# Performance work log

Measured on AMD Instinct MI355X. Metric: run time of the kernel, lower is better.

## Reference

```python
import jax, jax.numpy as jnp
import numpy as np

EMBEDDING_DIM = 256
NUM_EMBEDDINGS = 2048
COMMITMENT_COST = 0.25


def setup_inputs() -> dict:
    key = jax.random.key(0)
    k1, k2 = jax.random.split(key)
    inputs = jax.random.normal(k1, (32, EMBEDDING_DIM, 32, 32), dtype=jnp.float32)
    # learned codebook buffer, shape (D, K) as in the torch module
    embedding = jax.random.normal(k2, (EMBEDDING_DIM, NUM_EMBEDDINGS), dtype=jnp.float32)
    return {"inputs": inputs, "embedding": embedding}


def reference(inputs, embedding):
    # Eval-mode forward of VectorQuantizerEMA (EMA buffer updates are
    # training-only side effects and do not affect the returned values).
    B, D, H, W = inputs.shape
    K = embedding.shape[1]
    x = inputs.astype(jnp.float32)
    # (B, D, H, W) -> (N, D), N = B*H*W, clamped as in the source
    flat = jnp.clip(jnp.transpose(x, (0, 2, 3, 1)).reshape(-1, D), -10.0, 10.0)
    # squared L2 distances to every codeword: (N, K)
    distances = (
        jnp.sum(flat * flat, axis=1, keepdims=True)
        + jnp.sum(embedding * embedding, axis=0, keepdims=True)
        - 2.0 * (flat @ embedding)
    )
    encoding_indices = jnp.argmin(distances, axis=1)  # (N,)
    # one-hot @ emb.T is just a gather of codebook columns
    q_flat = jnp.take(embedding.T, encoding_indices, axis=0)  # (N, D)
    quantized = jnp.transpose(q_flat.reshape(B, H, W, D), (0, 3, 1, 2))
    # VQ losses (computed against the un-clamped float inputs, as in torch)
    e_latent_loss = jnp.mean((jax.lax.stop_gradient(quantized) - x) ** 2)
    q_latent_loss = jnp.mean((quantized - jax.lax.stop_gradient(x)) ** 2)
    loss = q_latent_loss + COMMITMENT_COST * e_latent_loss
    # straight-through estimator
    quantized_st = inputs + jax.lax.stop_gradient(quantized - inputs)
    # perplexity from codeword usage (mean one-hot == normalized counts)
    n = encoding_indices.shape[0]
    avg_probs = jnp.zeros((K,), dtype=jnp.float32).at[encoding_indices].add(1.0) / n
    perplexity = jnp.exp(-jnp.sum(avg_probs * jnp.log(avg_probs + 1e-10)))
    return quantized_st, loss, perplexity, encoding_indices
```

## Files before the change

kernel.cpp:

```cpp
#include <hip/hip_runtime.h>
#include <hip/hip_bf16.h>
#include <math.h>

typedef unsigned int  uint;
typedef unsigned short ushort;

#define DD    256
#define KK    2048
#define HW    1024
#define NN    32768
#define NUMEL 8388608
#define STRIDEB (DD*HW)
#define NBLK_QL (NUMEL/1024)

#define WS_H2     0
#define WS_COUNTS 8192
#define WS_LOSS   16384
#define WS_EBF    16512
#define WS_PV     2113664
#define WS_PI     2375808
#define WS_BPART  WS_PV

#define OUT_LOSS  8388608
#define OUT_PPL   8388609
#define OUT_IDX   8388610

typedef __attribute__((ext_vector_type(8))) short  short8;
typedef __attribute__((ext_vector_type(4))) float  float4v;

typedef __attribute__((address_space(1))) uint guint;
typedef __attribute__((address_space(3))) uint luint;

__device__ __forceinline__ ushort f2bf(float f) {
    uint u = __float_as_uint(f);
    return (ushort)((u + 0x7FFFu + ((u >> 16) & 1u)) >> 16);
}

__global__ __launch_bounds__(256) void e2h_kernel(const float* __restrict__ emb,
                                                  float* __restrict__ h2,
                                                  int*   __restrict__ counts) {
    int k = blockIdx.x * 256 + threadIdx.x;
    float s = 0.f;
    for (int d = 0; d < DD; ++d) {
        float v = emb[(size_t)d * KK + k];
        s += v * v;
    }
    h2[k] = 0.5f * s;
    counts[k] = 0;
}

__global__ __launch_bounds__(256) void prep_emb(const float* __restrict__ emb,
                                                ushort* __restrict__ ebf) {
    int g  = blockIdx.x * 256 + threadIdx.x;
    int k  = g & (KK - 1);
    int dg = g >> 11;
    int d0 = dg * 8;
    int s    = dg >> 2;
    int quad = dg & 3;
    int ct   = k >> 4;
    int l    = quad * 16 + (k & 15);

    union { ushort us[8]; uint4 v; } hu, lu;
#pragma unroll
    for (int j = 0; j < 8; ++j) {
        float v = emb[(size_t)(d0 + j) * KK + k];
        ushort hb = f2bf(v);
        float  hf = __uint_as_float(((uint)hb) << 16);
        hu.us[j] = hb;
        lu.us[j] = f2bf(v - hf);
    }
    size_t hi_off = (size_t)(((ct * 8 + s) * 2 + 0) * 64 + l) * 8;
    size_t lo_off = (size_t)(((ct * 8 + s) * 2 + 1) * 64 + l) * 8;
    *(uint4*)(ebf + hi_off) = hu.v;
    *(uint4*)(ebf + lo_off) = lu.v;
}

__global__ __launch_bounds__(256, 4) void argmin_mfma(
    const float*  __restrict__ x,
    const ushort* __restrict__ ebf,
    const float*  __restrict__ h2,
    float* __restrict__ pv,
    int*   __restrict__ pi)
{
    __shared__ ushort sB[2][8192];
    __shared__ float  sH2[1024];

    const int tid  = threadIdx.x;
    const int w    = tid >> 6;
    const int lane = tid & 63;
    const int m    = lane & 15;
    const int quad = lane >> 4;

    const int rb = blockIdx.x >> 1;
    const int ch = blockIdx.x & 1;
    const int n0 = rb * 64 + w * 16;
    const int b  = n0 >> 10;
    const int hwb = n0 & 1023;
    const float* xb = x + (size_t)b * STRIDEB;
    const int cbase = ch * 1024;
    const int ctg0  = cbase >> 4;

    auto stage = [&](ushort* dst, int ctg) {
        const char* gs = (const char*)(ebf + (size_t)ctg * 8192) + tid * 16;
        char*       ls = (char*)dst + tid * 16;
#pragma unroll
        for (int i = 0; i < 4; ++i)
            __builtin_amdgcn_global_load_lds((guint*)(gs + i * 4096),
                                             (luint*)(ls + i * 4096),
                                             16, 0, 0);
    };

    stage(sB[0], ctg0);
    ((float4*)sH2)[tid] = ((const float4*)(h2 + cbase))[tid];

    short8 xh[8], xl[8];
    {
        const int hw = hwb + m;
#pragma unroll
        for (int s = 0; s < 8; ++s) {
            const float* p = xb + (size_t)(s * 32 + quad * 8) * HW + hw;
            short8 hh, ll;
#pragma unroll
            for (int j = 0; j < 8; ++j) {
                float v = p[(size_t)j * HW];
                v = fminf(fmaxf(v, -10.f), 10.f);
                ushort hb = f2bf(v);
                float  hf = __uint_as_float(((uint)hb) << 16);
                hh[j] = (short)hb;
                ll[j] = (short)f2bf(v - hf);
            }
            xh[s] = hh;
            xl[s] = ll;
        }
    }

    float bv[4] = {1e30f, 1e30f, 1e30f, 1e30f};
    int   bi[4] = {0, 0, 0, 0};

    auto compute_tile = [&](const ushort* sbc, int ct) {
        float4v accA = {0,0,0,0}, accB = {0,0,0,0};
#pragma unroll
        for (int s = 0; s < 8; ++s) {
            short8 eh = *(const short8*)&sbc[(s * 2 + 0) * 512 + lane * 8];
            short8 el = *(const short8*)&sbc[(s * 2 + 1) * 512 + lane * 8];
            accB = __builtin_amdgcn_mfma_f32_16x16x32_bf16(xl[s], eh, accB, 0, 0, 0);
            accB = __builtin_amdgcn_mfma_f32_16x16x32_bf16(xh[s], el, accB, 0, 0, 0);
            accA = __builtin_amdgcn_mfma_f32_16x16x32_bf16(xh[s], eh, accA, 0, 0, 0);
        }
        const int c  = cbase + ct * 16 + m;
        const float hv = sH2[ct * 16 + m];
#pragma unroll
        for (int i = 0; i < 4; ++i) {
            float s0 = hv - (accA[i] + accB[i]);
            if (s0 < bv[i]) { bv[i] = s0; bi[i] = c; }
        }
    };

    __syncthreads();

    for (int ct = 0; ct < 64; ct += 2) {
        stage(sB[1], ctg0 + ct + 1);
        compute_tile(sB[0], ct);
        __syncthreads();
        stage(sB[0], (ct + 2 < 64) ? (ctg0 + ct + 2) : ctg0);
        compute_tile(sB[1], ct + 1);
        __syncthreads();
    }

#pragma unroll
    for (int i = 0; i < 4; ++i) {
        float v  = bv[i];
        int   ix = bi[i];
#pragma unroll
        for (int msk = 8; msk >= 1; msk >>= 1) {
            float ov = __shfl_xor(v, msk, 64);
            int   oi = __shfl_xor(ix, msk, 64);
            if (ov < v || (ov == v && oi < ix)) { v = ov; ix = oi; }
        }
        if (m == 0) {
            int n = n0 + quad * 4 + i;
            pv[n * 2 + ch] = v;
            pi[n * 2 + ch] = ix;
        }
    }
}

__global__ __launch_bounds__(256) void merge_kernel(
    const float* __restrict__ pv, const int* __restrict__ pi,
    float* __restrict__ out_idx_f, int* __restrict__ counts)
{
    int n = blockIdx.x * 256 + threadIdx.x;
    float v0 = pv[n * 2 + 0], v1 = pv[n * 2 + 1];
    int   i0 = pi[n * 2 + 0], i1 = pi[n * 2 + 1];
    int ix = (v1 < v0) ? i1 : i0;
    ix = min(max(ix, 0), KK - 1);
    out_idx_f[n] = (float)ix;
    atomicAdd(&counts[ix], 1);
}

__global__ __launch_bounds__(256) void quant_loss_kernel(
    const float* __restrict__ x,
    const float* __restrict__ emb,
    const float* __restrict__ idxf,
    float* __restrict__ outq,
    float* __restrict__ bpart)
{
    __shared__ float red[4];
    size_t o4 = ((size_t)blockIdx.x * 256 + threadIdx.x) * 4;
    int b  = (int)(o4 >> 18);
    int d  = (int)((o4 >> 10) & 255);
    int n  = b * HW + (int)(o4 & 1023);
    int i0 = (int)idxf[n + 0];
    int i1 = (int)idxf[n + 1];
    int i2 = (int)idxf[n + 2];
    int i3 = (int)idxf[n + 3];
    i0 = min(max(i0, 0), KK - 1); i1 = min(max(i1, 0), KK - 1);
    i2 = min(max(i2, 0), KK - 1); i3 = min(max(i3, 0), KK - 1);
    const float* er = emb + (size_t)d * KK;
    float4 q;
    q.x = er[i0]; q.y = er[i1]; q.z = er[i2]; q.w = er[i3];
    const float4 xv = *(const float4*)(x + o4);
    *(float4*)(outq + o4) = q;
    float ax = q.x - xv.x, ay = q.y - xv.y, az = q.z - xv.z, aw = q.w - xv.w;
    float s = ax * ax + ay * ay + az * az + aw * aw;
#pragma unroll
    for (int off = 32; off > 0; off >>= 1) s += __shfl_down(s, off, 64);
    if ((threadIdx.x & 63) == 0) red[threadIdx.x >> 6] = s;
    __syncthreads();
    if (threadIdx.x == 0)
        bpart[blockIdx.x] = red[0] + red[1] + red[2] + red[3];
}

__global__ __launch_bounds__(256) void finalize_kernel(
    const int* __restrict__ counts,
    const float* __restrict__ bpart,
    float* __restrict__ out)
{
    __shared__ float redp[4], redl[4];
    int tid = threadIdx.x;
    float s = 0.f;
    for (int k = tid; k < KK; k += 256) {
        float p = (float)counts[k] * (1.0f / (float)NN);
        s += p * logf(p + 1e-10f);
    }
    float ls = 0.f;
    for (int k = tid; k < NBLK_QL; k += 256) ls += bpart[k];
#pragma unroll
    for (int off = 32; off > 0; off >>= 1) {
        s  += __shfl_down(s, off, 64);
        ls += __shfl_down(ls, off, 64);
    }
    if ((tid & 63) == 0) { redp[tid >> 6] = s; redl[tid >> 6] = ls; }
    __syncthreads();
    if (tid == 0) {
        float tot = redp[0] + redp[1] + redp[2] + redp[3];
        float lsum = redl[0] + redl[1] + redl[2] + redl[3];
        out[OUT_PPL]  = expf(-tot);
        out[OUT_LOSS] = lsum * 1.25f / (float)NUMEL;
    }
}

extern "C" void kernel_launch(void* const* d_in, const int* in_sizes, int n_in,
                              void* d_out, int out_size, void* d_ws, size_t ws_size,
                              hipStream_t stream) {
    const float* x   = (const float*)d_in[0];
    const float* emb = (const float*)d_in[1];
    float* out = (float*)d_out;
    char*  ws  = (char*)d_ws;

    float*  h2     = (float*)(ws + WS_H2);
    int*    counts = (int*)(ws + WS_COUNTS);
    ushort* ebf    = (ushort*)(ws + WS_EBF);
    float*  pv     = (float*)(ws + WS_PV);
    int*    pi     = (int*)(ws + WS_PI);
    float*  bpart  = (float*)(ws + WS_BPART);

    e2h_kernel<<<KK / 256, 256, 0, stream>>>(emb, h2, counts);
    prep_emb<<<256, 256, 0, stream>>>(emb, ebf);
    argmin_mfma<<<1024, 256, 0, stream>>>(x, ebf, h2, pv, pi);
    merge_kernel<<<NN / 256, 256, 0, stream>>>(pv, pi, out + OUT_IDX, counts);
    quant_loss_kernel<<<NBLK_QL, 256, 0, stream>>>(x, emb, out + OUT_IDX, out, bpart);
    finalize_kernel<<<1, 256, 0, stream>>>(counts, bpart, out);
}
```

Measured before the change: 235.8 us.

## Triple-buffer codebook tiles with partial vmcnt waits and MFMA priority boost

```diff
diff --git a/kernel.cpp b/kernel.cpp
--- a/kernel.cpp
+++ b/kernel.cpp
@@ -82,7 +82,9 @@
     float* __restrict__ pv,
     int*   __restrict__ pi)
 {
-    __shared__ ushort sB[2][8192];
+    __shared__ ushort sB0[8192];
+    __shared__ ushort sB1[8192];
+    __shared__ ushort sB2[8192];
     __shared__ float  sH2[1024];
 
     const int tid  = threadIdx.x;
@@ -110,7 +112,8 @@
                                              16, 0, 0);
     };
 
-    stage(sB[0], ctg0);
+    stage(sB0, ctg0 + 0);
+    stage(sB1, ctg0 + 1);
     ((float4*)sH2)[tid] = ((const float4*)(h2 + cbase))[tid];
 
     short8 xh[8], xl[8];
@@ -156,16 +159,26 @@
         }
     };
 
+    auto step = [&](ushort* cbuf, ushort* nbuf, int t, int tn) {
+        stage(nbuf, ctg0 + tn);
+        asm volatile("s_waitcnt vmcnt(8)" ::: "memory");
+        __builtin_amdgcn_s_barrier();
+        __builtin_amdgcn_s_setprio(1);
+        compute_tile(cbuf, t);
+        __builtin_amdgcn_s_setprio(0);
+        __builtin_amdgcn_s_barrier();
+    };
+
     __syncthreads();
 
-    for (int ct = 0; ct < 64; ct += 2) {
-        stage(sB[1], ctg0 + ct + 1);
-        compute_tile(sB[0], ct);
-        __syncthreads();
-        stage(sB[0], (ct + 2 < 64) ? (ctg0 + ct + 2) : ctg0);
-        compute_tile(sB[1], ct + 1);
-        __syncthreads();
-    }
+    for (int t = 0; t < 63; t += 3) {
+        step(sB0, sB2, t,     t + 2);
+        step(sB1, sB0, t + 1, t + 3);
+        step(sB2, sB1, t + 2, (t + 4 < 64) ? t + 4 : 0);
+    }
+    asm volatile("s_waitcnt vmcnt(4)" ::: "memory");
+    __builtin_amdgcn_s_barrier();
+    compute_tile(sB0, 63);
 
 #pragma unroll
     for (int i = 0; i < 4; ++i) {
```

New measurement: 242.1 us. +2.6%, slower.
